# Performance work log

Measured on AMD Instinct MI355X. Metric: run time of the kernel, lower is better.

## Reference

```python
import jax, jax.numpy as jnp
import numpy as np

N, C, H, W = 32, 512, 32, 32
S = 2048
INFLUENCE = 1.0  # influence_decay='constant', training_progress irrelevant


def setup_inputs() -> dict:
    key = jax.random.key(0)
    k1, k2 = jax.random.split(key)
    x = jax.random.normal(k1, (N, C, H, W), dtype=jnp.float32)
    # nn.Parameter(torch.randn(S, C) / C)
    codebook = jax.random.normal(k2, (S, C), dtype=jnp.float32) / C
    return {"x": x, "codebook": codebook}


def _distances(x_flat, codebook):
    # x_flat: [N, C, P], codebook: [S, C] -> [N, S, P]
    # same math as ((x[:,None]-cb[None,...,None])**2).sum(2), without the
    # [N, S, C, P] intermediate
    x2 = jnp.sum(x_flat * x_flat, axis=1)          # [N, P]
    c2 = jnp.sum(codebook * codebook, axis=1)      # [S]
    xc = jnp.einsum('ncp,sc->nsp', x_flat, codebook)  # [N, S, P]
    return x2[:, None, :] + c2[None, :, None] - 2.0 * xc


def reference(x, codebook):
    n, c = x.shape[:2]
    x_flat = x.reshape(n, c, -1)                      # [N, C, P]
    xs = jax.lax.stop_gradient(x_flat)                # distance(x_flat.detach())
    d = _distances(xs, codebook)                      # [N, S, P]
    idx = jnp.argmin(d, axis=1)                       # [N, P]
    xq = jnp.transpose(codebook[idx], (0, 2, 1)).reshape(x.shape)  # [N,C,H,W]
    loss_commitment = jnp.mean((x - jax.lax.stop_gradient(xq)) ** 2)
    d_sorted = jnp.sort(d, axis=1)                    # ascending over S
    w = jnp.exp(-jnp.arange(d.shape[1], dtype=jnp.float32) / INFLUENCE)
    loss_codebook = jnp.mean(w[None, :, None] * d_sorted)
    codebook_indices = idx.reshape(n, *x.shape[2:])   # [N, H, W]
    output = x + jax.lax.stop_gradient(xq - x)        # straight-through
    return (loss_codebook, loss_commitment, codebook_indices, output)
```

## Files before the change

kernel.cpp:

```cpp
#include <hip/hip_runtime.h>
#include <hip/hip_fp16.h>

#define N_ 32
#define C_ 512
#define P_ 1024
#define S_ 2048
#define NR_ (N_ * P_)
#define GUARD 6e-3f
#define TSIG 2.3f

typedef __attribute__((ext_vector_type(8))) short sh8;
typedef __attribute__((ext_vector_type(4))) float fx4;

#define WS_XT       0ull
#define WS_XTF      33554432ull
#define WS_CBT      100663296ull
#define WS_C2F      102760448ull
#define WS_X2       102768640ull
#define WS_CNT      102899712ull
#define WS_CANDV    103030784ull
#define WS_CANDS    111419392ull
#define WS_ROWPART  119808000ull
#define WS_COMMIT   120070144ull
#define WS_TOTAL    120201216ull

#define TBLK 1024
#define CVTBLK 512

__device__ __forceinline__ unsigned short f2bf(float f) {
  union { float f; unsigned u; } x; x.f = f;
  unsigned r = x.u + 0x7fffu + ((x.u >> 16) & 1u);
  return (unsigned short)(r >> 16);
}

template <typename T>
__device__ __forceinline__ void load16_lds(const T* g, T* l) {
  __builtin_amdgcn_global_load_lds((const __attribute__((address_space(1))) void*)g,
                                   (__attribute__((address_space(3))) void*)l, 16, 0, 0);
}

__global__ __launch_bounds__(256) void k_prep(const float* __restrict__ x,
                                              const float* __restrict__ cb,
                                              unsigned short* __restrict__ xT,
                                              float* __restrict__ xTf,
                                              unsigned short* __restrict__ cbT,
                                              float* __restrict__ c2f,
                                              float* __restrict__ x2ws,
                                              int* __restrict__ cnt) {
  __shared__ float tile[32][260];
  const int tid = threadIdx.x;
  const int bx = blockIdx.x;

  if (bx < TBLK) {
    const int n = bx >> 5;
    const int p0 = (bx & 31) << 5;
    const float* xb = x + (size_t)n * (C_ * P_) + p0;
    const int p4 = (tid & 7) << 2;
    const int ch = tid >> 3;

    float acc = 0.f;
#pragma unroll
    for (int pass = 0; pass < 2; ++pass) {
      if (pass) __syncthreads();
#pragma unroll
      for (int it = 0; it < 8; ++it) {
        int cl = (it << 5) + ch;
        float4 v = *(const float4*)(xb + (size_t)(pass * 256 + cl) * P_ + p4);
        tile[p4 + 0][cl] = v.x;
        tile[p4 + 1][cl] = v.y;
        tile[p4 + 2][cl] = v.z;
        tile[p4 + 3][cl] = v.w;
      }
      __syncthreads();

#pragma unroll
      for (int it = 0; it < 8; ++it) {
        int idx = tid + 256 * it;
        int row = idx >> 6, c4 = (idx & 63) << 2;
        float4 f = *(const float4*)&tile[row][c4];
        size_t R = (size_t)((n << 10) + p0 + row);
        size_t cg = (size_t)pass * 256 + c4;
        *(float4*)(xTf + R * C_ + cg) = f;
        ushort4 o;
        o.x = f2bf(f.x); o.y = f2bf(f.y); o.z = f2bf(f.z); o.w = f2bf(f.w);
        *(ushort4*)(xT + R * C_ + cg) = o;
      }

      if (tid < 32) {
        for (int c = 0; c < 256; ++c) {
          float t = tile[tid][c];
          acc = __fadd_rn(acc, __fmul_rn(t, t));
        }
      }
    }
    if (tid < 32) {
      int R = (n << 10) + p0 + tid;
      x2ws[R] = acc;
      cnt[R] = 0;
    }
  } else {
    const int s = (bx - TBLK) * 4 + (tid >> 6);
    const int l = tid & 63;
    const float* row = cb + (size_t)s * C_;
    double c2d = 0.0;
#pragma unroll
    for (int h = 0; h < 2; ++h) {
      int c = h * 256 + l * 4;
      float4 v = *(const float4*)(row + c);
      ushort4 o;
      o.x = f2bf(v.x); o.y = f2bf(v.y); o.z = f2bf(v.z); o.w = f2bf(v.w);
      *(ushort4*)(cbT + (size_t)s * C_ + c) = o;
      c2d += (double)__fmul_rn(v.x, v.x) + (double)__fmul_rn(v.y, v.y) +
             (double)__fmul_rn(v.z, v.z) + (double)__fmul_rn(v.w, v.w);
    }
#pragma unroll
    for (int off = 32; off > 0; off >>= 1) c2d += __shfl_down(c2d, off);
    if (l == 0) c2f[s] = (float)c2d;
  }
}

__global__ __launch_bounds__(256, 4) void k_gemm(const unsigned short* __restrict__ xT,
                                                 const unsigned short* __restrict__ cbT,
                                                 const float* __restrict__ x2ws,
                                                 float* __restrict__ candv,
                                                 int* __restrict__ cands,
                                                 int* __restrict__ cnt) {
  __shared__ unsigned short As[128 * 64];
  __shared__ unsigned short Bs[128 * 64];
  __shared__ float t_lds[128];
  const int tid = threadIdx.x;
  const int w = tid >> 6, l = tid & 63;
  const int bx = blockIdx.x;
  const int m_tile = ((bx >> 7) << 3) + (bx & 7);
  const int s_tile = (bx >> 3) & 15;
  const int m0 = m_tile << 7, s0 = s_tile << 7;
  const int wm = (w & 1) << 6, wsf = (w >> 1) << 6;
  const int quad = l >> 4, lane15 = l & 15;

  if (tid < 128) t_lds[tid] = TSIG * __fsqrt_rn(x2ws[m0 + tid]) * (1.0f / 512.0f);

  size_t gA[4], gB[4];
  unsigned short *lA[4], *lB[4];
#pragma unroll
  for (int q = 0; q < 4; ++q) {
    int chunk = (q * 4 + w) * 64 + l;
    int m = chunk >> 3, k8s = chunk & 7;
    int k8 = k8s ^ (m & 7);
    gA[q] = (size_t)(m0 + m) * (C_ * 2) + (size_t)k8 * 16;
    gB[q] = (size_t)(s0 + m) * (C_ * 2) + (size_t)k8 * 16;
    lA[q] = As + (q * 4 + w) * 512;
    lB[q] = Bs + (q * 4 + w) * 512;
  }
  const char* xb = (const char*)xT;
  const char* cbb = (const char*)cbT;

  fx4 acc[4][4];
#pragma unroll
  for (int i = 0; i < 4; ++i)
#pragma unroll
    for (int j = 0; j < 4; ++j) acc[i][j] = (fx4){0.f, 0.f, 0.f, 0.f};

  for (int kk = 0; kk < 8; ++kk) {
#pragma unroll
    for (int q = 0; q < 4; ++q) {
      load16_lds((const unsigned short*)(xb + gA[q] + (size_t)kk * 128), lA[q]);
      load16_lds((const unsigned short*)(cbb + gB[q] + (size_t)kk * 128), lB[q]);
    }
    __syncthreads();
#pragma unroll
    for (int ks = 0; ks < 2; ++ks) {
      const int k8g = ks * 4 + quad;
      sh8 af[4], bf[4];
#pragma unroll
      for (int mi = 0; mi < 4; ++mi) {
        int m = wm + mi * 16 + lane15;
        af[mi] = *(const sh8*)(As + m * 64 + (k8g ^ (m & 7)) * 8);
      }
#pragma unroll
      for (int si = 0; si < 4; ++si) {
        int s = wsf + si * 16 + lane15;
        bf[si] = *(const sh8*)(Bs + s * 64 + (k8g ^ (s & 7)) * 8);
      }
#pragma unroll
      for (int mi = 0; mi < 4; ++mi)
#pragma unroll
        for (int si = 0; si < 4; ++si)
          acc[mi][si] = __builtin_amdgcn_mfma_f32_16x16x32_bf16(af[mi], bf[si], acc[mi][si], 0, 0, 0);
    }
    __syncthreads();
  }

  const unsigned below = (1u << lane15) - 1u;
#pragma unroll
  for (int mi = 0; mi < 4; ++mi) {
#pragma unroll
    for (int r = 0; r < 4; ++r) {
      const int rowl = wm + mi * 16 + quad * 4 + r;
      const int rowg = m0 + rowl;
      const float t = t_lds[rowl];
      float v[4]; int scol[4]; bool hit[4];
      float vmax = -1e30f; int smax = 0;
#pragma unroll
      for (int si = 0; si < 4; ++si) {
        v[si] = acc[mi][si][r];
        scol[si] = s0 + wsf + si * 16 + lane15;
        hit[si] = v[si] >= t;
        if (v[si] > vmax) { vmax = v[si]; smax = scol[si]; }
      }
      int total = 0, myslot[4];
#pragma unroll
      for (int si = 0; si < 4; ++si) {
        unsigned long long b = __ballot(hit[si]);
        unsigned seg = (unsigned)((b >> (quad * 16)) & 0xFFFFull);
        myslot[si] = total + __popc(seg & below);
        total += __popc(seg);
      }
#pragma unroll
      for (int off = 1; off < 16; off <<= 1) {
        float ov = __shfl_xor(vmax, off);
        int os = __shfl_xor(smax, off);
        if (ov > vmax) { vmax = ov; smax = os; }
      }
      int base = 0;
      if (lane15 == 0) base = atomicAdd(&cnt[rowg], total > 0 ? total : 1);
      base = __shfl(base, quad * 16);
      if (total > 0) {
#pragma unroll
        for (int si = 0; si < 4; ++si) {
          if (hit[si]) {
            int slot = base + myslot[si];
            if (slot < 64) {
              candv[(size_t)rowg * 64 + slot] = v[si];
              cands[(size_t)rowg * 64 + slot] = scol[si];
            }
          }
        }
      } else if (lane15 == 0 && base < 64) {
        candv[(size_t)rowg * 64 + base] = vmax;
        cands[(size_t)rowg * 64 + base] = smax;
      }
    }
  }
}

__global__ __launch_bounds__(256, 4) void k_phase2(
    const float* __restrict__ cb, const float* __restrict__ xTf,
    const float* __restrict__ candvG, const int* __restrict__ candsG,
    const int* __restrict__ cntG, const float* __restrict__ c2f,
    const float* __restrict__ x2ws, float* __restrict__ out,
    double* __restrict__ rowpart) {
  __shared__ float xrow[4][C_];
  const int tid = threadIdx.x;
  const int w = tid >> 6, l = tid & 63;
  const int R = blockIdx.x * 4 + w;

  const int cnt = min(cntG[R], 64);
  const float x2f = x2ws[R];
  const bool act = l < cnt;
  float v = candvG[(size_t)R * 64 + l];
  int s = candsG[(size_t)R * 64 + l];
  v = act ? v : -1e30f;
  s = act ? s : 0x7fffffff;
  const int sIdx = act ? s : 0;
  const float dt = act
      ? __fsub_rn(__fadd_rn(x2f, c2f[sIdx]), __fmul_rn(2.f, v))
      : 1e30f;

  float M = v;
#pragma unroll
  for (int off = 1; off < 64; off <<= 1) M = fmaxf(M, __shfl_xor(M, off));

  int rank = 0;
  for (int k = 0; k < 64; ++k) {
    float dk = __shfl(dt, k);
    int sk = __shfl(s, k);
    rank += (dk < dt || (dk == dt && sk < s)) ? 1 : 0;
  }

  double contrib = act ? (double)__expf(-(float)rank) * (double)dt : 0.0;
#pragma unroll
  for (int off = 32; off > 0; off >>= 1) contrib += __shfl_down(contrib, off);
  if (l == 0) rowpart[R] = contrib;

  const bool near = act && (v >= M - GUARD);
  const unsigned long long bal = __ballot(near);
  const int nres = __popcll(bal);
  if (nres == 1) {
    int src = __ffsll(bal) - 1;
    int wins = __shfl(s, src);
    if (l == 0) out[2 + R] = (float)wins;
  } else {
#pragma unroll
    for (int k = 0; k < 2; ++k)
      *(float4*)&xrow[w][l * 8 + k * 4] = *(const float4*)(xTf + (size_t)R * C_ + l * 8 + k * 4);
    float d32 = 1e30f;
    if (near) {
      const float4* crow = (const float4*)(cb + (size_t)s * C_);
      float acc = 0.f;
#pragma unroll 8
      for (int i = 0; i < C_ / 4; ++i) {
        float4 cv = crow[i];
        float4 xv = *(const float4*)&xrow[w][i * 4];
        acc = __fadd_rn(acc, __fmul_rn(xv.x, cv.x));
        acc = __fadd_rn(acc, __fmul_rn(xv.y, cv.y));
        acc = __fadd_rn(acc, __fmul_rn(xv.z, cv.z));
        acc = __fadd_rn(acc, __fmul_rn(xv.w, cv.w));
      }
      d32 = __fsub_rn(__fadd_rn(x2f, c2f[s]), __fmul_rn(2.f, acc));
    }
    float bd = d32;
    int bs2 = near ? s : 0x7fffffff;
#pragma unroll
    for (int off = 1; off < 64; off <<= 1) {
      float ov = __shfl_xor(bd, off);
      int os = __shfl_xor(bs2, off);
      if (ov < bd || (ov == bd && os < bs2)) { bd = ov; bs2 = os; }
    }
    if (l == 0) out[2 + R] = (float)bs2;
  }
}

__global__ __launch_bounds__(256) void k2_output(
    const float* __restrict__ x, const float* __restrict__ cb,
    float* __restrict__ out, double* __restrict__ commit_partial) {
  __shared__ double r2[4];
  const int tid = threadIdx.x;
  const int bx = blockIdx.x;
  const int n = bx >> 9, c = bx & 511;
  const int p = tid * 4;

  const float* xr = x + ((size_t)n * C_ + c) * P_ + p;
  float4 xv = *(const float4*)xr;
  float xs[4] = {xv.x, xv.y, xv.z, xv.w};
  const float* idxf = out + 2 + n * P_ + p;
  float o[4];
  float acc = 0.f;
#pragma unroll
  for (int k = 0; k < 4; ++k) {
    int s = (int)idxf[k];
    float q = cb[(size_t)s * C_ + c];
    float t = __fsub_rn(q, xs[k]);
    o[k] = __fadd_rn(xs[k], t);
    float dd = __fsub_rn(xs[k], q);
    acc += dd * dd;
  }
  float* orow = out + 2 + N_ * P_ + ((size_t)n * C_ + c) * P_ + p;
  ((float2*)orow)[0] = make_float2(o[0], o[1]);
  ((float2*)orow)[1] = make_float2(o[2], o[3]);

  double dacc = (double)acc;
#pragma unroll
  for (int off = 32; off > 0; off >>= 1) dacc += __shfl_down(dacc, off);
  if ((tid & 63) == 0) r2[tid >> 6] = dacc;
  __syncthreads();
  if (tid == 0) commit_partial[bx] = r2[0] + r2[1] + r2[2] + r2[3];
}

__global__ __launch_bounds__(256) void k3_finalize(
    const double* __restrict__ pa, int na, const double* __restrict__ pb, int nb,
    float* __restrict__ out) {
  __shared__ double red[8];
  const int tid = threadIdx.x;
  double a = 0.0, b = 0.0;
  for (int i = tid; i < na; i += 256) a += pa[i];
  for (int i = tid; i < nb; i += 256) b += pb[i];
#pragma unroll
  for (int off = 32; off > 0; off >>= 1) {
    a += __shfl_down(a, off);
    b += __shfl_down(b, off);
  }
  if ((tid & 63) == 0) {
    red[(tid >> 6) * 2 + 0] = a;
    red[(tid >> 6) * 2 + 1] = b;
  }
  __syncthreads();
  if (tid == 0) {
    double A = red[0] + red[2] + red[4] + red[6];
    double B = red[1] + red[3] + red[5] + red[7];
    out[0] = (float)(A / ((double)N_ * (double)S_ * (double)P_));
    out[1] = (float)(B / ((double)N_ * (double)C_ * (double)P_));
  }
}

#define TPW 8
#define KC 32
#define SC 64
#define KCF 48
__global__ __launch_bounds__(256) void k1_fallback(
    const float* __restrict__ x, const float* __restrict__ cb,
    float* __restrict__ out, double* __restrict__ cb_partial) {
  __shared__ float dval[TPW][KCF];
  __shared__ float x2f[TPW];
  __shared__ double redd[4];
  __shared__ float x_t[TPW][C_ + 4];
  __shared__ float cb_t[SC][KC + 4];
  __shared__ int cand_s[TPW][KCF];
  __shared__ _Float16 sc[S_][TPW];

  const int tid = threadIdx.x;
  const int bx = blockIdx.x;
  const int n = bx >> 7;
  const int p0 = (bx & 127) * TPW;

  const float* xn = x + (size_t)n * C_ * P_ + p0;
#pragma unroll
  for (int q = 0; q < 16; ++q) {
    int e = tid + 256 * q;
    int c = e >> 3, j = e & 7;
    x_t[j][c] = xn[(size_t)c * P_ + j];
  }
  __syncthreads();
  if (tid < TPW) {
    float acc = 0.f;
    for (int c = 0; c < C_; ++c)
      acc = __fadd_rn(acc, __fmul_rn(x_t[tid][c], x_t[tid][c]));
    x2f[tid] = acc;
  }
  const int j = tid & 7;
  const int sg = tid >> 3;
  for (int s0 = 0; s0 < S_; s0 += SC) {
    float acc0 = 0.f, acc1 = 0.f;
    for (int k0 = 0; k0 < C_; k0 += KC) {
      __syncthreads();
#pragma unroll
      for (int q = 0; q < 8; ++q) {
        int e = tid + 256 * q;
        int i = e >> 5, cc = e & 31;
        cb_t[i][cc] = cb[(size_t)(s0 + i) * C_ + k0 + cc];
      }
      __syncthreads();
      const float* xr = &x_t[j][k0];
#pragma unroll
      for (int cs = 0; cs < KC; cs += 4) {
        float4 xv = *(const float4*)(xr + cs);
        float4 a4 = *(const float4*)(&cb_t[sg][cs]);
        float4 b4 = *(const float4*)(&cb_t[sg + 32][cs]);
        acc0 += xv.x * a4.x + xv.y * a4.y + xv.z * a4.z + xv.w * a4.w;
        acc1 += xv.x * b4.x + xv.y * b4.y + xv.z * b4.z + xv.w * b4.w;
      }
    }
    sc[s0 + sg][j] = (_Float16)acc0;
    sc[s0 + sg + 32][j] = (_Float16)acc1;
  }
  __syncthreads();
  {
    const int g = tid >> 5, t = tid & 31;
    for (int pass = 0; pass < KCF; ++pass) {
      float bv = -1e30f;
      int bs = 0;
      for (int k = 0; k < 64; ++k) {
        int s = t + 32 * k;
        float vv = (float)sc[s][g];
        if (vv > bv) { bv = vv; bs = s; }
      }
#pragma unroll
      for (int off = 1; off < 32; off <<= 1) {
        float ov = __shfl_xor(bv, off);
        int os = __shfl_xor(bs, off);
        if (ov > bv || (ov == bv && os < bs)) { bv = ov; bs = os; }
      }
      if (t == 0) {
        cand_s[g][pass] = bs;
        sc[bs][g] = (_Float16)(-65504.f);
      }
      __syncthreads();
    }
  }
  for (int task = tid; task < TPW * KCF; task += 256) {
    int jj = task / KCF, r = task % KCF;
    int s = cand_s[jj][r];
    const float* row = cb + (size_t)s * C_;
    const float* xrw = &x_t[jj][0];
    float acc = 0.f;
    double c2d = 0.0;
    for (int c = 0; c < C_; c += 4) {
      float4 cv = *(const float4*)(row + c);
      acc = __fadd_rn(acc, __fmul_rn(xrw[c + 0], cv.x));
      acc = __fadd_rn(acc, __fmul_rn(xrw[c + 1], cv.y));
      acc = __fadd_rn(acc, __fmul_rn(xrw[c + 2], cv.z));
      acc = __fadd_rn(acc, __fmul_rn(xrw[c + 3], cv.w));
      c2d += (double)__fmul_rn(cv.x, cv.x);
      c2d += (double)__fmul_rn(cv.y, cv.y);
      c2d += (double)__fmul_rn(cv.z, cv.z);
      c2d += (double)__fmul_rn(cv.w, cv.w);
    }
    float c2s = (float)c2d;
    dval[jj][r] = __fsub_rn(__fadd_rn(x2f[jj], c2s), __fmul_rn(2.f, acc));
  }
  __syncthreads();
  double contrib = 0.0;
  for (int task = tid; task < TPW * KCF; task += 256) {
    int jj = task / KCF, r = task % KCF;
    float e = dval[jj][r];
    int s = cand_s[jj][r];
    int rank = 0;
    for (int r2 = 0; r2 < KCF; ++r2) {
      float e2 = dval[jj][r2];
      int s2 = cand_s[jj][r2];
      rank += (e2 < e || (e2 == e && s2 < s)) ? 1 : 0;
    }
    contrib += exp((double)(-rank)) * (double)e;
    if (rank == 0) out[2 + n * P_ + p0 + jj] = (float)s;
  }
  __syncthreads();
#pragma unroll
  for (int off = 32; off > 0; off >>= 1) contrib += __shfl_down(contrib, off);
  if ((tid & 63) == 0) redd[tid >> 6] = contrib;
  __syncthreads();
  if (tid == 0) cb_partial[bx] = redd[0] + redd[1] + redd[2] + redd[3];
}

extern "C" void kernel_launch(void* const* d_in, const int* in_sizes, int n_in,
                              void* d_out, int out_size, void* d_ws, size_t ws_size,
                              hipStream_t stream) {
  const float* x = (const float*)d_in[0];
  const float* cb = (const float*)d_in[1];
  float* out = (float*)d_out;
  char* ws = (char*)d_ws;

  if (ws_size >= WS_TOTAL) {
    unsigned short* xT = (unsigned short*)(ws + WS_XT);
    float* xTf = (float*)(ws + WS_XTF);
    unsigned short* cbT = (unsigned short*)(ws + WS_CBT);
    float* c2f = (float*)(ws + WS_C2F);
    float* x2ws = (float*)(ws + WS_X2);
    int* cnt = (int*)(ws + WS_CNT);
    float* candv = (float*)(ws + WS_CANDV);
    int* cands = (int*)(ws + WS_CANDS);
    double* rowpart = (double*)(ws + WS_ROWPART);
    double* commitp = (double*)(ws + WS_COMMIT);

    hipLaunchKernelGGL(k_prep, dim3(TBLK + CVTBLK), dim3(256), 0, stream,
                       x, cb, xT, xTf, cbT, c2f, x2ws, cnt);
    hipLaunchKernelGGL(k_gemm, dim3(4096), dim3(256), 0, stream,
                       xT, cbT, x2ws, candv, cands, cnt);
    hipLaunchKernelGGL(k_phase2, dim3(NR_ / 4), dim3(256), 0, stream,
                       cb, xTf, candv, cands, cnt, c2f, x2ws, out, rowpart);
    hipLaunchKernelGGL(k2_output, dim3(16384), dim3(256), 0, stream, x, cb, out, commitp);
    hipLaunchKernelGGL(k3_finalize, dim3(1), dim3(256), 0, stream,
                       rowpart, NR_, commitp, 16384, out);
  } else {
    double* cb_partial = (double*)d_ws;
    double* commitp = cb_partial + 4096;
    hipLaunchKernelGGL(k1_fallback, dim3(4096), dim3(256), 0, stream, x, cb, out, cb_partial);
    hipLaunchKernelGGL(k2_output, dim3(16384), dim3(256), 0, stream, x, cb, out, commitp);
    hipLaunchKernelGGL(k3_finalize, dim3(1), dim3(256), 0, stream,
                       cb_partial, 4096, commitp, 16384, out);
  }
}
```

Measured before the change: 473.1 us.

## Stage codebook rows in LDS for output gather and pack candidate value/index pairs

The output kernel now handles 16 pixels by 512 channels per block. It loads the 16 selected codebook rows into LDS with contiguous float4 reads, replacing the scattered per-element gathers from cb, and writes output as float4. Candidate value and index pairs are packed into one uint2 array, so the gemm and phase2 kernels each do one 8-byte access per candidate instead of two separate array accesses. The cost is fewer, larger blocks (2048 instead of 16384) and LDS staging with two syncs per block.

Result: faster. 432.8 us (-8.5%).

```diff
diff --git a/kernel.cpp b/kernel.cpp
--- a/kernel.cpp
+++ b/kernel.cpp
@@ -18,8 +18,7 @@
 #define WS_C2F      102760448ull
 #define WS_X2       102768640ull
 #define WS_CNT      102899712ull
-#define WS_CANDV    103030784ull
-#define WS_CANDS    111419392ull
+#define WS_CAND     103030784ull
 #define WS_ROWPART  119808000ull
 #define WS_COMMIT   120070144ull
 #define WS_TOTAL    120201216ull
@@ -122,8 +121,7 @@
 __global__ __launch_bounds__(256, 4) void k_gemm(const unsigned short* __restrict__ xT,
                                                  const unsigned short* __restrict__ cbT,
                                                  const float* __restrict__ x2ws,
-                                                 float* __restrict__ candv,
-                                                 int* __restrict__ cands,
+                                                 uint2* __restrict__ cand,
                                                  int* __restrict__ cnt) {
   __shared__ unsigned short As[128 * 64];
   __shared__ unsigned short Bs[128 * 64];
@@ -230,14 +228,14 @@
           if (hit[si]) {
             int slot = base + myslot[si];
             if (slot < 64) {
-              candv[(size_t)rowg * 64 + slot] = v[si];
-              cands[(size_t)rowg * 64 + slot] = scol[si];
+              cand[(size_t)rowg * 64 + slot] =
+                  make_uint2(__float_as_uint(v[si]), (unsigned)scol[si]);
             }
           }
         }
       } else if (lane15 == 0 && base < 64) {
-        candv[(size_t)rowg * 64 + base] = vmax;
-        cands[(size_t)rowg * 64 + base] = smax;
+        cand[(size_t)rowg * 64 + base] =
+            make_uint2(__float_as_uint(vmax), (unsigned)smax);
       }
     }
   }
@@ -245,7 +243,7 @@
 
 __global__ __launch_bounds__(256, 4) void k_phase2(
     const float* __restrict__ cb, const float* __restrict__ xTf,
-    const float* __restrict__ candvG, const int* __restrict__ candsG,
+    const uint2* __restrict__ candG,
     const int* __restrict__ cntG, const float* __restrict__ c2f,
     const float* __restrict__ x2ws, float* __restrict__ out,
     double* __restrict__ rowpart) {
@@ -257,8 +255,9 @@
   const int cnt = min(cntG[R], 64);
   const float x2f = x2ws[R];
   const bool act = l < cnt;
-  float v = candvG[(size_t)R * 64 + l];
-  int s = candsG[(size_t)R * 64 + l];
+  uint2 ce = candG[(size_t)R * 64 + l];
+  float v = __uint_as_float(ce.x);
+  int s = (int)ce.y;
   v = act ? v : -1e30f;
   s = act ? s : 0x7fffffff;
   const int sIdx = act ? s : 0;
@@ -323,32 +322,50 @@
 __global__ __launch_bounds__(256) void k2_output(
     const float* __restrict__ x, const float* __restrict__ cb,
     float* __restrict__ out, double* __restrict__ commit_partial) {
+  __shared__ float qt[16][516];
+  __shared__ int s_lds[16];
   __shared__ double r2[4];
   const int tid = threadIdx.x;
   const int bx = blockIdx.x;
-  const int n = bx >> 9, c = bx & 511;
-  const int p = tid * 4;
-
-  const float* xr = x + ((size_t)n * C_ + c) * P_ + p;
-  float4 xv = *(const float4*)xr;
-  float xs[4] = {xv.x, xv.y, xv.z, xv.w};
-  const float* idxf = out + 2 + n * P_ + p;
-  float o[4];
-  float acc = 0.f;
-#pragma unroll
-  for (int k = 0; k < 4; ++k) {
-    int s = (int)idxf[k];
-    float q = cb[(size_t)s * C_ + c];
-    float t = __fsub_rn(q, xs[k]);
-    o[k] = __fadd_rn(xs[k], t);
-    float dd = __fsub_rn(xs[k], q);
-    acc += dd * dd;
-  }
-  float* orow = out + 2 + N_ * P_ + ((size_t)n * C_ + c) * P_ + p;
-  ((float2*)orow)[0] = make_float2(o[0], o[1]);
-  ((float2*)orow)[1] = make_float2(o[2], o[3]);
-
-  double dacc = (double)acc;
+  const int n = bx >> 6;
+  const int p0 = (bx & 63) << 4;
+
+  if (tid < 16) s_lds[tid] = (int)out[2 + n * P_ + p0 + tid];
+  __syncthreads();
+  {
+    const int p = tid >> 4, c0 = (tid & 15) << 2;
+    const float* row = cb + (size_t)s_lds[p] * C_;
+#pragma unroll
+    for (int it = 0; it < 8; ++it) {
+      int c = c0 + (it << 6);
+      *(float4*)&qt[p][c] = *(const float4*)(row + c);
+    }
+  }
+  __syncthreads();
+
+  const int cl = tid >> 2, pq = (tid & 3) << 2;
+  double dacc = 0.0;
+#pragma unroll
+  for (int chunk = 0; chunk < 8; ++chunk) {
+    int c = (chunk << 6) + cl;
+    const float* xr = x + ((size_t)n * C_ + c) * P_ + p0 + pq;
+    float4 xv = *(const float4*)xr;
+    float xs[4] = {xv.x, xv.y, xv.z, xv.w};
+    float o[4];
+    float acc = 0.f;
+#pragma unroll
+    for (int k = 0; k < 4; ++k) {
+      float q = qt[pq + k][c];
+      float t = __fsub_rn(q, xs[k]);
+      o[k] = __fadd_rn(xs[k], t);
+      float dd = __fsub_rn(xs[k], q);
+      acc += dd * dd;
+    }
+    float* orow = out + 2 + N_ * P_ + ((size_t)n * C_ + c) * P_ + p0 + pq;
+    *(float4*)orow = make_float4(o[0], o[1], o[2], o[3]);
+    dacc += (double)acc;
+  }
+
 #pragma unroll
   for (int off = 32; off > 0; off >>= 1) dacc += __shfl_down(dacc, off);
   if ((tid & 63) == 0) r2[tid >> 6] = dacc;
@@ -525,26 +542,25 @@
     float* c2f = (float*)(ws + WS_C2F);
     float* x2ws = (float*)(ws + WS_X2);
     int* cnt = (int*)(ws + WS_CNT);
-    float* candv = (float*)(ws + WS_CANDV);
-    int* cands = (int*)(ws + WS_CANDS);
+    uint2* cand = (uint2*)(ws + WS_CAND);
     double* rowpart = (double*)(ws + WS_ROWPART);
     double* commitp = (double*)(ws + WS_COMMIT);
 
     hipLaunchKernelGGL(k_prep, dim3(TBLK + CVTBLK), dim3(256), 0, stream,
                        x, cb, xT, xTf, cbT, c2f, x2ws, cnt);
     hipLaunchKernelGGL(k_gemm, dim3(4096), dim3(256), 0, stream,
-                       xT, cbT, x2ws, candv, cands, cnt);
+                       xT, cbT, x2ws, cand, cnt);
     hipLaunchKernelGGL(k_phase2, dim3(NR_ / 4), dim3(256), 0, stream,
-                       cb, xTf, candv, cands, cnt, c2f, x2ws, out, rowpart);
-    hipLaunchKernelGGL(k2_output, dim3(16384), dim3(256), 0, stream, x, cb, out, commitp);
+                       cb, xTf, cand, cnt, c2f, x2ws, out, rowpart);
+    hipLaunchKernelGGL(k2_output, dim3(2048), dim3(256), 0, stream, x, cb, out, commitp);
     hipLaunchKernelGGL(k3_finalize, dim3(1), dim3(256), 0, stream,
-                       rowpart, NR_, commitp, 16384, out);
+                       rowpart, NR_, commitp, 2048, out);
   } else {
     double* cb_partial = (double*)d_ws;
     double* commitp = cb_partial + 4096;
     hipLaunchKernelGGL(k1_fallback, dim3(4096), dim3(256), 0, stream, x, cb, out, cb_partial);
-    hipLaunchKernelGGL(k2_output, dim3(16384), dim3(256), 0, stream, x, cb, out, commitp);
+    hipLaunchKernelGGL(k2_output, dim3(2048), dim3(256), 0, stream, x, cb, out, commitp);
     hipLaunchKernelGGL(k3_finalize, dim3(1), dim3(256), 0, stream,
-                       cb_partial, 4096, commitp, 16384, out);
-  }
-}
+                       cb_partial, 4096, commitp, 2048, out);
+  }
+}
```
